# Optimization experiments

Measured on AMD Instinct MI355X. Metric: run time of the kernel, lower is better.

The kernel has to match this reference:

```python
import jax, jax.numpy as jnp
import numpy as np

N, E, H, B = 100000, 1600000, 64, 256
EPS = 1e-5


def ln(x, g, b):
    mu = jnp.mean(x, axis=-1, keepdims=True)
    var = jnp.mean((x - mu) ** 2, axis=-1, keepdims=True)
    return (x - mu) * jax.lax.rsqrt(var + EPS) * g + b


def gelu(x):
    # torch nn.GELU default is exact (erf) gelu
    return jax.nn.gelu(x, approximate=False)


def setup_inputs() -> dict:
    key = jax.random.key(0)
    ks = iter(jax.random.split(key, 64))
    nk = lambda: next(ks)
    s = 0.1
    p = {}
    p["x"] = jax.random.normal(nk(), (N, 2), jnp.float32)
    p["edge_attr"] = jax.random.normal(nk(), (E, 2), jnp.float32)
    # node_embed: Linear(2,H) LN GELU Linear(H,H) LN GELU (dropout = eval no-op)
    p["ne_w1"] = jax.random.normal(nk(), (2, H), jnp.float32) * s
    p["ne_b1"] = jnp.zeros((H,), jnp.float32)
    p["ne_g1"] = jnp.ones((H,), jnp.float32)
    p["ne_be1"] = jnp.zeros((H,), jnp.float32)
    p["ne_w2"] = jax.random.normal(nk(), (H, H), jnp.float32) * s
    p["ne_b2"] = jnp.zeros((H,), jnp.float32)
    p["ne_g2"] = jnp.ones((H,), jnp.float32)
    p["ne_be2"] = jnp.zeros((H,), jnp.float32)
    # 3 TrackConv layers: message MLP Linear(H+2,H)+LN, conv output LN, and outer per-layer LN
    p["conv_w"] = jax.random.normal(nk(), (3, H + 2, H), jnp.float32) * s
    p["conv_b"] = jnp.zeros((3, H), jnp.float32)
    p["conv_mg"] = jnp.ones((3, H), jnp.float32)
    p["conv_mb"] = jnp.zeros((3, H), jnp.float32)
    p["conv_ng"] = jnp.ones((3, H), jnp.float32)
    p["conv_nb"] = jnp.zeros((3, H), jnp.float32)
    p["out_ng"] = jnp.ones((3, H), jnp.float32)
    p["out_nb"] = jnp.zeros((3, H), jnp.float32)
    # head MLP: Linear(H,H)+LN+ReLU, Linear(H,H//2)+LN+ReLU, Linear(H//2,1)
    p["m_w1"] = jax.random.normal(nk(), (H, H), jnp.float32) * s
    p["m_b1"] = jnp.zeros((H,), jnp.float32)
    p["m_g1"] = jnp.ones((H,), jnp.float32)
    p["m_be1"] = jnp.zeros((H,), jnp.float32)
    p["m_w2"] = jax.random.normal(nk(), (H, H // 2), jnp.float32) * s
    p["m_b2"] = jnp.zeros((H // 2,), jnp.float32)
    p["m_g2"] = jnp.ones((H // 2,), jnp.float32)
    p["m_be2"] = jnp.zeros((H // 2,), jnp.float32)
    p["m_w3"] = jax.random.normal(nk(), (H // 2, 1), jnp.float32) * s
    p["m_b3"] = jnp.zeros((1,), jnp.float32)
    p["edge_index"] = jax.random.randint(nk(), (2, E), 0, N, dtype=jnp.int32)
    p["batch"] = jnp.sort(jax.random.randint(nk(), (N,), 0, B, dtype=jnp.int32))
    return p


def reference(x, edge_attr,
              ne_w1, ne_b1, ne_g1, ne_be1, ne_w2, ne_b2, ne_g2, ne_be2,
              conv_w, conv_b, conv_mg, conv_mb, conv_ng, conv_nb, out_ng, out_nb,
              m_w1, m_b1, m_g1, m_be1, m_w2, m_b2, m_g2, m_be2, m_w3, m_b3,
              edge_index, batch):
    # node embedding (dropout in eval = identity)
    h = gelu(ln(x @ ne_w1 + ne_b1, ne_g1, ne_be1))
    h = gelu(ln(h @ ne_w2 + ne_b2, ne_g2, ne_be2))
    src, dst = edge_index[0], edge_index[1]  # PyG: message from src (x_j), aggregate at dst
    deg = jax.ops.segment_sum(jnp.ones((E,), h.dtype), dst, num_segments=N)
    deg = jnp.maximum(deg, 1.0)[:, None]
    for l in range(3):
        msg_in = jnp.concatenate([h[src], edge_attr], axis=-1)  # [E, H+2]
        msg = gelu(ln(msg_in @ conv_w[l] + conv_b[l], conv_mg[l], conv_mb[l]))  # [E, H]
        agg = jax.ops.segment_sum(msg, dst, num_segments=N) / deg  # mean aggregate
        conv_out = ln(agg + h, conv_ng[l], conv_nb[l])  # TrackConv: norm(out + residual)
        h = h + ln(conv_out, out_ng[l], out_nb[l])  # outer norm + residual
    # global mean pool over graphs
    cnt = jnp.maximum(jax.ops.segment_sum(jnp.ones((N,), h.dtype), batch, num_segments=B), 1.0)[:, None]
    g = jax.ops.segment_sum(h, batch, num_segments=B) / cnt  # [B, H]
    g = jax.nn.relu(ln(g @ m_w1 + m_b1, m_g1, m_be1))
    g = jax.nn.relu(ln(g @ m_w2 + m_b2, m_g2, m_be2))
    return g @ m_w3 + m_b3  # [B, 1]
```

## Files before the change

### kernel.cpp

```cpp
#include <hip/hip_runtime.h>
#include <math.h>


typedef __attribute__((ext_vector_type(8))) short bfrag;
typedef __attribute__((ext_vector_type(4))) float ffrag;

template <int CTRL>
__device__ __forceinline__ float dpp_mov(float v) {
  return __int_as_float(
      __builtin_amdgcn_update_dpp(0, __float_as_int(v), CTRL, 0xF, 0xF, true));
}

__device__ __forceinline__ float rsum16(float v) {
  v += dpp_mov<0x128>(v);
  v += dpp_mov<0x124>(v);
  v += dpp_mov<0x122>(v);
  v += dpp_mov<0x121>(v);
  return v;
}

__device__ __forceinline__ float wave_sum64(float v) {
  v = rsum16(v);
  v += __shfl_xor(v, 16, 64);
  v += __shfl_xor(v, 32, 64);
  return v;
}

__device__ __forceinline__ float ln_apply(float t, float g, float b) {
  float s1 = wave_sum64(t);
  float s2 = wave_sum64(t * t);
  float mu = s1 * 0.015625f;
  float var = fmaf(-mu, mu, s2 * 0.015625f);
  return (t - mu) * rsqrtf(var + 1e-5f) * g + b;
}

__device__ __forceinline__ float erf_fast(float x) {
  float ax = fabsf(x);
  float p = fmaf(fmaf(fmaf(fmaf(0.078108f, ax, 0.000972f), ax, 0.230389f),
                      ax, 0.278393f), ax, 1.0f);
  p = p * p;
  p = p * p;
  float r = __builtin_amdgcn_rcpf(p);
  return copysignf(1.0f - r, x);
}

__device__ __forceinline__ float gelu_exact(float v) {
  float half = 0.5f * v;
  return fmaf(half, erf_fast(v * 0.70710678118654752440f), half);
}

__device__ __forceinline__ float lane_bcast(float v, int k) {
  return __uint_as_float(__builtin_amdgcn_readlane(__float_as_uint(v), k));
}

__device__ __forceinline__ short f2bf(float f) {
  union { float f; unsigned u; } v; v.f = f;
  unsigned r = v.u + 0x7fffu + ((v.u >> 16) & 1u);
  return (short)(r >> 16);
}

__global__ __launch_bounds__(256) void k_init1(
    const float* __restrict__ conv_w, ushort* __restrict__ wt,
    const int* __restrict__ ei, int* __restrict__ csr,
    int ne, int oHist) {
  const int bid = blockIdx.x;
  const int tid = threadIdx.x;
  if (bid < oHist) {
    const int i = bid * 256 + tid;
    const int k = i % 96, f = (i / 96) % 64, l = i / (96 * 64);
    const float v = (k < 66) ? conv_w[(size_t)l * 66 * 64 + k * 64 + f] : 0.0f;
    wt[i] = (ushort)f2bf(v);
    return;
  }
  const int i = (bid - oHist) * 256 + tid;
  if (i < ne) atomicAdd(&csr[__builtin_nontemporal_load(ei + ne + i)], 1);
}

__global__ __launch_bounds__(1024) void k_scan_fast(int* __restrict__ buf, int n) {
  __shared__ int wsum[16];
  const int tid = threadIdx.x, lane = tid & 63, w = tid >> 6;
  const int chunk = (((n + 1023) / 1024) + 3) & ~3;
  const int a = min(tid * chunk, n), b = min(a + chunk, n);
  const bool full = (a + chunk <= n);
  int s = 0;
  if (full) {
    const int4* p4 = (const int4*)(buf + a);
#pragma unroll 4
    for (int i = 0; i < chunk / 4; i++) {
      int4 v = p4[i];
      s += v.x + v.y + v.z + v.w;
    }
  } else {
    for (int i = a; i < b; i++) s += buf[i];
  }
  int inc = s;
#pragma unroll
  for (int sh = 1; sh < 64; sh <<= 1) {
    int t = __shfl_up(inc, sh, 64);
    if (lane >= sh) inc += t;
  }
  if (lane == 63) wsum[w] = inc;
  __syncthreads();
  int wb = 0;
  for (int j = 0; j < w; j++) wb += wsum[j];
  int excl = wb + inc - s;
  if (full) {
    int4* p4 = (int4*)(buf + a);
#pragma unroll 4
    for (int i = 0; i < chunk / 4; i++) {
      int4 v = p4[i];
      int4 o;
      o.x = excl; excl += v.x;
      o.y = excl; excl += v.y;
      o.z = excl; excl += v.z;
      o.w = excl; excl += v.w;
      p4[i] = o;
    }
  } else {
    for (int i = a; i < b; i++) { int v = buf[i]; buf[i] = excl; excl += v; }
  }
}

__global__ __launch_bounds__(256) void k_combo(
    const int* __restrict__ ei, const float* __restrict__ ea,
    int* __restrict__ cursor, int4* __restrict__ edata,
    const float* __restrict__ x,
    const float* __restrict__ w1, const float* __restrict__ b1,
    const float* __restrict__ g1, const float* __restrict__ be1,
    const float* __restrict__ w2, const float* __restrict__ b2,
    const float* __restrict__ g2, const float* __restrict__ be2,
    float* __restrict__ h, ushort* __restrict__ hb,
    int n_nodes, int ne, int nOrd, int embWaves, float roleScale) {
  const int bid = blockIdx.x;
  const int tid = threadIdx.x;
  const int sub = bid & 31;
  if (sub < 24) {
    const int role = bid & 7;
    const int ord = (bid >> 5) * 3 + (sub >> 3);
    const int lo = (int)((long long)ord * ne / nOrd);
    const int hi = (int)((long long)(ord + 1) * ne / nOrd);
    for (int i = lo + tid; i < hi; i += 256) {
      const int d = __builtin_nontemporal_load(ei + ne + i);
      const int rd = min(7, (int)((float)d * roleScale));
      if (rd == role) {
        const int s = __builtin_nontemporal_load(ei + i);
        const unsigned long long eau =
            __builtin_nontemporal_load((const unsigned long long*)ea + i);
        const float e0 = __uint_as_float((unsigned)eau);
        const float e1 = __uint_as_float((unsigned)(eau >> 32));
        const unsigned pk = (unsigned)(ushort)f2bf(e0) |
                            ((unsigned)(ushort)f2bf(e1) << 16);
        const int pos = atomicAdd(&cursor[d], 1);
        edata[pos] = make_int4(s, (int)pk, d, 0);
      }
    }
    return;
  }
  const int lane = tid & 63;
  const int eblk = (bid >> 5) * 8 + (sub - 24);
  const int wid = (eblk * 256 + tid) >> 6;
  const int nw = embWaves;
  float wc[64];
#pragma unroll
  for (int k = 0; k < 64; k++) wc[k] = w2[k * 64 + lane];
  const float w1a = w1[lane], w1b = w1[64 + lane];
  const float vb1 = b1[lane], vg1 = g1[lane], vbe1 = be1[lane];
  const float vb2 = b2[lane], vg2 = g2[lane], vbe2 = be2[lane];
  for (int n = wid; n < n_nodes; n += nw) {
    const float x0 = x[2 * n], x1 = x[2 * n + 1];
    float t = fmaf(x0, w1a, fmaf(x1, w1b, vb1));
    t = gelu_exact(ln_apply(t, vg1, vbe1));
    float a0 = vb2, a1 = 0.f, a2 = 0.f, a3 = 0.f;
#pragma unroll
    for (int k = 0; k < 64; k += 4) {
      a0 = fmaf(lane_bcast(t, k + 0), wc[k + 0], a0);
      a1 = fmaf(lane_bcast(t, k + 1), wc[k + 1], a1);
      a2 = fmaf(lane_bcast(t, k + 2), wc[k + 2], a2);
      a3 = fmaf(lane_bcast(t, k + 3), wc[k + 3], a3);
    }
    float acc = (a0 + a1) + (a2 + a3);
    acc = gelu_exact(ln_apply(acc, vg2, vbe2));
    __builtin_nontemporal_store(acc, h + (size_t)n * 64 + lane);
    __builtin_nontemporal_store((ushort)f2bf(acc),
                                hb + (size_t)n * 64 + lane);
  }
}

__global__ __launch_bounds__(256, 3) void k_edge_packed(
    const ushort* __restrict__ hb_in, float* __restrict__ agg,
    const int4* __restrict__ edata, const ushort* __restrict__ wt,
    const float* __restrict__ bias, const float* __restrict__ mg,
    const float* __restrict__ mb, int nchunks, int ne) {
  __shared__ __align__(16) ushort lwt[64 * 96];
  {
    const uint4* s = (const uint4*)wt;
    uint4* d = (uint4*)lwt;
    for (int i = threadIdx.x; i < 768; i += 256) d[i] = s[i];
  }
  __syncthreads();

  const int lane = threadIdx.x & 63;
  const int grp = lane >> 4, col = lane & 15;
  const int wid = (blockIdx.x * blockDim.x + threadIdx.x) >> 6;
  const int nw = (gridDim.x * blockDim.x) >> 6;

  float vb[4], vg[4], vbb[4];
#pragma unroll
  for (int t = 0; t < 4; t++) {
    const int f = t * 16 + col;
    vb[t] = bias[f]; vg[t] = mg[f]; vbb[t] = mb[f];
  }

  int c = wid;
  if (c >= nchunks) return;
  int4 e = edata[min(16 * c + col, ne - 1)];
  const ushort* hp0 = hb_in + (size_t)e.x * 64 + grp * 8;
  bfrag A0 = *(const bfrag*)(hp0);
  bfrag A1 = *(const bfrag*)(hp0 + 32);

  for (;;) {
    const int rem = min(16, ne - 16 * c);
    const int cn = c + nw;
    const bool more = cn < nchunks;
    const int nslot = more ? min(16 * cn + col, ne - 1) : min(16 * c + col, ne - 1);
    const int4 en = edata[nslot];

    bfrag A2 = {0, 0, 0, 0, 0, 0, 0, 0};
    if (grp == 0) {
      A2[0] = (short)(e.y & 0xffff);
      A2[1] = (short)((unsigned)e.y >> 16);
    }

    ffrag acc[4];
#pragma unroll
    for (int t = 0; t < 4; t++) { ffrag cc = {vb[t], vb[t], vb[t], vb[t]}; acc[t] = cc; }
#pragma unroll
    for (int t = 0; t < 4; t++) {
      const bfrag B = *(const bfrag*)(lwt + (t * 16 + col) * 96 + grp * 8);
      acc[t] = __builtin_amdgcn_mfma_f32_16x16x32_bf16(A0, B, acc[t], 0, 0, 0);
    }
#pragma unroll
    for (int t = 0; t < 4; t++) {
      const bfrag B = *(const bfrag*)(lwt + (t * 16 + col) * 96 + 32 + grp * 8);
      acc[t] = __builtin_amdgcn_mfma_f32_16x16x32_bf16(A1, B, acc[t], 0, 0, 0);
    }
#pragma unroll
    for (int t = 0; t < 4; t++) {
      const bfrag B = *(const bfrag*)(lwt + (t * 16 + col) * 96 + 64 + grp * 8);
      acc[t] = __builtin_amdgcn_mfma_f32_16x16x32_bf16(A2, B, acc[t], 0, 0, 0);
    }

    const ushort* hq = hb_in + (size_t)en.x * 64 + grp * 8;
    const bfrag N0 = *(const bfrag*)(hq);
    const bfrag N1 = *(const bfrag*)(hq + 32);

    float sx[4], sq[4];
#pragma unroll
    for (int r = 0; r < 4; r++) {
      float s = (acc[0][r] + acc[1][r]) + (acc[2][r] + acc[3][r]);
      float q = fmaf(acc[0][r], acc[0][r], fmaf(acc[1][r], acc[1][r],
                fmaf(acc[2][r], acc[2][r], acc[3][r] * acc[3][r])));
      sx[r] = s; sq[r] = q;
    }
#pragma unroll
    for (int r = 0; r < 4; r++) sx[r] = rsum16(sx[r]);
#pragma unroll
    for (int r = 0; r < 4; r++) sq[r] = rsum16(sq[r]);
    float iv[4], mi[4];
#pragma unroll
    for (int r = 0; r < 4; r++) {
      const float mu = sx[r] * 0.015625f;
      const float var = fmaf(-mu, mu, sq[r] * 0.015625f);
      iv[r] = rsqrtf(var + 1e-5f);
      mi[r] = -mu * iv[r];
    }

#pragma unroll
    for (int t = 0; t < 4; t++) {
#pragma unroll
      for (int r = 0; r < 4; r++) {
        const float z = fmaf(acc[t][r], iv[r], mi[r]);
        acc[t][r] = gelu_exact(fmaf(z, vg[t], vbb[t]));
      }
    }

    const int prev = __shfl_up(e.z, 1, 64);
    const unsigned long long bal = __ballot((col > 0) && (e.z != prev));
    const unsigned bm = (unsigned)bal & 0xFFFEu;

    int s0 = 0;
    while (s0 < rem) {
      const unsigned rest = bm >> (s0 + 1);
      int s1 = rest ? (s0 + 1 + __builtin_ctz(rest)) : 16;
      if (s1 > rem) s1 = rem;
      const int dseg = __builtin_amdgcn_readlane(e.z, s0);
#pragma unroll
      for (int t = 0; t < 4; t++) {
        float rs = 0.f;
#pragma unroll
        for (int r = 0; r < 4; r++) {
          const int row = grp * 4 + r;
          const float w = (row >= s0 && row < s1) ? 1.0f : 0.0f;
          rs = fmaf(acc[t][r], w, rs);
        }
        rs += __shfl_xor(rs, 16, 64);
        rs += __shfl_xor(rs, 32, 64);
        if (lane < 16)
          atomicAdd(&agg[(size_t)dseg * 64 + t * 16 + lane], rs);
      }
      s0 = s1;
    }

    if (!more) break;
    c = cn; e = en; A0 = N0; A1 = N1;
  }
}

__global__ void k_node_update(float* __restrict__ h, ushort* __restrict__ hb,
                              float* __restrict__ agg, const int* __restrict__ ends,
                              const float* __restrict__ ng, const float* __restrict__ nb,
                              const float* __restrict__ og, const float* __restrict__ ob,
                              int n_nodes, int writeHb) {
  const int lane = threadIdx.x & 63;
  const int n = (blockIdx.x * blockDim.x + threadIdx.x) >> 6;
  if (n >= n_nodes) return;
  int start, end;
  if (n == 0) { start = 0; end = ends[0]; }
  else { const int2 se = *(const int2*)(ends + n - 1); start = se.x; end = se.y; }
  const float dg = fmaxf((float)(end - start), 1.0f);
  const float hv = h[(size_t)n * 64 + lane];
  const float a = agg[(size_t)n * 64 + lane] / dg + hv;
  if (writeHb) agg[(size_t)n * 64 + lane] = 0.0f;
  const float c = ln_apply(a, ng[lane], nb[lane]);
  const float o = ln_apply(c, og[lane], ob[lane]);
  const float outv = hv + o;
  h[(size_t)n * 64 + lane] = outv;
  if (writeHb) hb[(size_t)n * 64 + lane] = (ushort)f2bf(outv);
}

__global__ void k_pool_seg(const float* __restrict__ h, const int* __restrict__ batch,
                           float* __restrict__ g, float* __restrict__ cnt,
                           int n_nodes, int chunk) {
  const int lane = threadIdx.x & 63;
  const int wid = (blockIdx.x * blockDim.x + threadIdx.x) >> 6;
  const int n0 = wid * chunk;
  if (n0 >= n_nodes) return;
  const int n1 = min(n0 + chunk, n_nodes);
  int cur = batch[n0], c = 0;
  float acc = 0.f;
  for (int n = n0; n < n1; n++) {
    const int b = batch[n];
    if (b != cur) {
      atomicAdd(&g[(size_t)cur * 64 + lane], acc);
      if (lane == 0) atomicAdd(&cnt[cur], (float)c);
      acc = 0.f; c = 0; cur = b;
    }
    acc += h[(size_t)n * 64 + lane];
    c++;
  }
  atomicAdd(&g[(size_t)cur * 64 + lane], acc);
  if (lane == 0) atomicAdd(&cnt[cur], (float)c);
}

__global__ void k_head(const float* __restrict__ g, const float* __restrict__ cnt,
                       const float* __restrict__ w1, const float* __restrict__ b1,
                       const float* __restrict__ g1, const float* __restrict__ be1,
                       const float* __restrict__ w2, const float* __restrict__ b2,
                       const float* __restrict__ g2, const float* __restrict__ be2,
                       const float* __restrict__ w3, const float* __restrict__ b3,
                       float* __restrict__ out, int nb_) {
  const int lane = threadIdx.x & 63;
  const int row = (blockIdx.x * blockDim.x + threadIdx.x) >> 6;
  if (row >= nb_) return;
  const float c = fmaxf(cnt[row], 1.0f);
  const float gv = g[row * 64 + lane] / c;
  float a0 = b1[lane], a1 = 0.f, a2 = 0.f, a3 = 0.f;
#pragma unroll
  for (int k = 0; k < 64; k += 4) {
    a0 = fmaf(lane_bcast(gv, k + 0), w1[(k + 0) * 64 + lane], a0);
    a1 = fmaf(lane_bcast(gv, k + 1), w1[(k + 1) * 64 + lane], a1);
    a2 = fmaf(lane_bcast(gv, k + 2), w1[(k + 2) * 64 + lane], a2);
    a3 = fmaf(lane_bcast(gv, k + 3), w1[(k + 3) * 64 + lane], a3);
  }
  float t = (a0 + a1) + (a2 + a3);
  t = fmaxf(ln_apply(t, g1[lane], be1[lane]), 0.0f);

  const int j = lane & 31;
  float c0 = b2[j], c1 = 0.f, c2 = 0.f, c3 = 0.f;
#pragma unroll
  for (int k = 0; k < 64; k += 4) {
    c0 = fmaf(lane_bcast(t, k + 0), w2[(k + 0) * 32 + j], c0);
    c1 = fmaf(lane_bcast(t, k + 1), w2[(k + 1) * 32 + j], c1);
    c2 = fmaf(lane_bcast(t, k + 2), w2[(k + 2) * 32 + j], c2);
    c3 = fmaf(lane_bcast(t, k + 3), w2[(k + 3) * 32 + j], c3);
  }
  float t2 = (c0 + c1) + (c2 + c3);
  t2 = fmaxf(ln_apply(t2, g2[j], be2[j]), 0.0f);
  const float p = t2 * w3[j];
  const float s = wave_sum64(p) * 0.5f;
  if (lane == 0) out[row] = s + b3[0];
}

extern "C" void kernel_launch(void* const* d_in, const int* in_sizes, int n_in,
                              void* d_out, int out_size, void* d_ws, size_t ws_size,
                              hipStream_t stream) {
  const float* x      = (const float*)d_in[0];
  const float* ea     = (const float*)d_in[1];
  const float* ne_w1  = (const float*)d_in[2];
  const float* ne_b1  = (const float*)d_in[3];
  const float* ne_g1  = (const float*)d_in[4];
  const float* ne_be1 = (const float*)d_in[5];
  const float* ne_w2  = (const float*)d_in[6];
  const float* ne_b2  = (const float*)d_in[7];
  const float* ne_g2  = (const float*)d_in[8];
  const float* ne_be2 = (const float*)d_in[9];
  const float* conv_w = (const float*)d_in[10];
  const float* conv_b = (const float*)d_in[11];
  const float* conv_mg= (const float*)d_in[12];
  const float* conv_mb= (const float*)d_in[13];
  const float* conv_ng= (const float*)d_in[14];
  const float* conv_nb= (const float*)d_in[15];
  const float* out_ng = (const float*)d_in[16];
  const float* out_nb = (const float*)d_in[17];
  const float* m_w1   = (const float*)d_in[18];
  const float* m_b1   = (const float*)d_in[19];
  const float* m_g1   = (const float*)d_in[20];
  const float* m_be1  = (const float*)d_in[21];
  const float* m_w2   = (const float*)d_in[22];
  const float* m_b2   = (const float*)d_in[23];
  const float* m_g2   = (const float*)d_in[24];
  const float* m_be2  = (const float*)d_in[25];
  const float* m_w3   = (const float*)d_in[26];
  const float* m_b3   = (const float*)d_in[27];
  const int*   eidx   = (const int*)d_in[28];
  const int*   batch  = (const int*)d_in[29];
  float* outp = (float*)d_out;

  const int NN = in_sizes[29];
  const int NE = in_sizes[1] / 2;
  const int NB = out_size;
  const int NCH = (NE + 15) / 16;

  char* wsb = (char*)d_ws;
  float*  h    = (float*)wsb;
  ushort* hb   = (ushort*)(h + (size_t)NN * 64);
  int4*   edata= (int4*)((char*)hb + ((size_t)NN * 128 + 15) / 16 * 16);
  ushort* wt   = (ushort*)(edata + NE);
  float*  gbuf = (float*)(wt + 3 * 64 * 96);
  float*  cnt  = gbuf + (size_t)NB * 64;
  int*    csr  = (int*)(cnt + NB);
  float*  agg  = (float*)((char*)(csr + NN) +
                          (((size_t)(uintptr_t)(csr + NN) & 15) ? 16 - ((size_t)(uintptr_t)(csr + NN) & 15) : 0));

  const dim3 blk(256);

  const size_t zbytes = (char*)(agg + (size_t)NN * 64) - (char*)gbuf;
  hipMemsetAsync(gbuf, 0, zbytes, stream);

  const int nPrep = (3 * 64 * 96) / 256;
  const int nHist = (NE + 255) / 256;
  k_init1<<<nPrep + nHist, blk, 0, stream>>>(conv_w, wt, eidx, csr, NE, nPrep);

  k_scan_fast<<<1, 1024, 0, stream>>>(csr, NN);

  const int ngroups = 261;
  const int nOrd = ngroups * 3;
  const int nEmb = ngroups * 8;
  k_combo<<<ngroups * 32, blk, 0, stream>>>(
      eidx, ea, csr, edata, x,
      ne_w1, ne_b1, ne_g1, ne_be1, ne_w2, ne_b2, ne_g2, ne_be2,
      h, hb, NN, NE, nOrd, nEmb * 4, 8.0f / (float)NN);

  for (int l = 0; l < 3; l++) {
    k_edge_packed<<<4096, blk, 0, stream>>>(
        hb, agg, edata, wt + (size_t)l * 64 * 96,
        conv_b + l * 64, conv_mg + l * 64, conv_mb + l * 64, NCH, NE);
    k_node_update<<<(NN * 64 + 255) / 256, blk, 0, stream>>>(
        h, hb, agg, csr, conv_ng + l * 64, conv_nb + l * 64,
        out_ng + l * 64, out_nb + l * 64, NN, (l < 2) ? 1 : 0);
  }

  {
    const int chunk = 32;
    const int nwaves = (NN + chunk - 1) / chunk;
    const int nblocks = (nwaves * 64 + 255) / 256;
    k_pool_seg<<<nblocks, blk, 0, stream>>>(h, batch, gbuf, cnt, NN, chunk);
  }
  k_head<<<(NB + 3) / 4, blk, 0, stream>>>(gbuf, cnt, m_w1, m_b1, m_g1, m_be1,
                                           m_w2, m_b2, m_g2, m_be2, m_w3, m_b3,
                                           outp, NB);
}
```

Before: 744.6 us.

## Partition edges by destination node ranges to replace atomics with plain stores

Each wave now owns a contiguous range of destination nodes, found by binary search over the CSR offsets, so the edges it processes are split at node boundaries. Partial sums for a destination that spans chunks are carried in registers and written once with a plain store instead of atomicAdd. This drops the float atomics and the zeroing of the aggregation buffer each layer, and the memset no longer covers agg. In exchange, work per wave is uneven when node degrees are skewed, and each wave pays for two binary searches.

```diff
diff --git a/kernel.cpp b/kernel.cpp
--- a/kernel.cpp
+++ b/kernel.cpp
@@ -4,6 +4,8 @@
 
 typedef __attribute__((ext_vector_type(8))) short bfrag;
 typedef __attribute__((ext_vector_type(4))) float ffrag;
+
+#define NWV 16384
 
 template <int CTRL>
 __device__ __forceinline__ float dpp_mov(float v) {
@@ -57,6 +59,16 @@
   union { float f; unsigned u; } v; v.f = f;
   unsigned r = v.u + 0x7fffu + ((v.u >> 16) & 1u);
   return (short)(r >> 16);
+}
+
+__device__ __forceinline__ int ub_search(const int* __restrict__ a, int n,
+                                         long long T) {
+  int lo = 0, hi = n;
+  while (lo < hi) {
+    const int mid = (lo + hi) >> 1;
+    if ((long long)a[mid] > T) hi = mid; else lo = mid + 1;
+  }
+  return lo;
 }
 
 __global__ __launch_bounds__(256) void k_init1(
@@ -186,11 +198,12 @@
   }
 }
 
-__global__ __launch_bounds__(256, 3) void k_edge_packed(
+__global__ __launch_bounds__(256, 3) void k_edge_seq(
     const ushort* __restrict__ hb_in, float* __restrict__ agg,
-    const int4* __restrict__ edata, const ushort* __restrict__ wt,
+    const int4* __restrict__ edata, const int* __restrict__ csr,
+    const ushort* __restrict__ wt,
     const float* __restrict__ bias, const float* __restrict__ mg,
-    const float* __restrict__ mb, int nchunks, int ne) {
+    const float* __restrict__ mb, int nn, int ne) {
   __shared__ __align__(16) ushort lwt[64 * 96];
   {
     const uint4* s = (const uint4*)wt;
@@ -200,9 +213,18 @@
   __syncthreads();
 
   const int lane = threadIdx.x & 63;
+  const int wgl = (int)((blockIdx.x * blockDim.x + threadIdx.x) >> 6);
+  const long long Ta = (long long)wgl * ne / NWV;
+  const long long Tb = (long long)(wgl + 1) * ne / NWV;
+  const int n0 = ub_search(csr, nn, Ta);
+  const int n1 = (wgl + 1 == NWV) ? nn : ub_search(csr, nn, Tb);
+  if (n0 >= n1) return;
+  const int e_lo = (n0 > 0) ? csr[n0 - 1] : 0;
+  const int e_hi = csr[n1 - 1];
+  const int nch = (e_hi - e_lo + 15) >> 4;
+  if (nch == 0) return;
+
   const int grp = lane >> 4, col = lane & 15;
-  const int wid = (blockIdx.x * blockDim.x + threadIdx.x) >> 6;
-  const int nw = (gridDim.x * blockDim.x) >> 6;
 
   float vb[4], vg[4], vbb[4];
 #pragma unroll
@@ -211,18 +233,18 @@
     vb[t] = bias[f]; vg[t] = mg[f]; vbb[t] = mb[f];
   }
 
-  int c = wid;
-  if (c >= nchunks) return;
-  int4 e = edata[min(16 * c + col, ne - 1)];
+  float car[4] = {0.f, 0.f, 0.f, 0.f};
+
+  int slot = min(e_lo + col, e_hi - 1);
+  int4 e = edata[slot];
   const ushort* hp0 = hb_in + (size_t)e.x * 64 + grp * 8;
   bfrag A0 = *(const bfrag*)(hp0);
   bfrag A1 = *(const bfrag*)(hp0 + 32);
 
-  for (;;) {
-    const int rem = min(16, ne - 16 * c);
-    const int cn = c + nw;
-    const bool more = cn < nchunks;
-    const int nslot = more ? min(16 * cn + col, ne - 1) : min(16 * c + col, ne - 1);
+  for (int c = 0;;) {
+    const int rem = min(16, e_hi - e_lo - 16 * c);
+    const bool more = (c + 1) < nch;
+    const int nslot = more ? min(e_lo + 16 * (c + 1) + col, e_hi - 1) : slot;
     const int4 en = edata[nslot];
 
     bfrag A2 = {0, 0, 0, 0, 0, 0, 0, 0};
@@ -287,6 +309,7 @@
     const int prev = __shfl_up(e.z, 1, 64);
     const unsigned long long bal = __ballot((col > 0) && (e.z != prev));
     const unsigned bm = (unsigned)bal & 0xFFFEu;
+    const int peek = more ? __builtin_amdgcn_readlane(en.z, 0) : -1;
 
     int s0 = 0;
     while (s0 < rem) {
@@ -294,30 +317,44 @@
       int s1 = rest ? (s0 + 1 + __builtin_ctz(rest)) : 16;
       if (s1 > rem) s1 = rem;
       const int dseg = __builtin_amdgcn_readlane(e.z, s0);
+
+      float rs[4];
 #pragma unroll
       for (int t = 0; t < 4; t++) {
-        float rs = 0.f;
+        float r_ = 0.f;
 #pragma unroll
         for (int r = 0; r < 4; r++) {
           const int row = grp * 4 + r;
           const float w = (row >= s0 && row < s1) ? 1.0f : 0.0f;
-          rs = fmaf(acc[t][r], w, rs);
+          r_ = fmaf(acc[t][r], w, r_);
         }
-        rs += __shfl_xor(rs, 16, 64);
-        rs += __shfl_xor(rs, 32, 64);
-        if (lane < 16)
-          atomicAdd(&agg[(size_t)dseg * 64 + t * 16 + lane], rs);
+        r_ += __shfl_xor(r_, 16, 64);
+        r_ += __shfl_xor(r_, 32, 64);
+        rs[t] = r_;
+      }
+
+      const bool comp = (s1 < rem) || (!more) || (peek != dseg);
+      if (comp) {
+        if (lane < 16) {
+#pragma unroll
+          for (int t = 0; t < 4; t++)
+            agg[(size_t)dseg * 64 + t * 16 + lane] = car[t] + rs[t];
+        }
+        car[0] = car[1] = car[2] = car[3] = 0.f;
+      } else {
+#pragma unroll
+        for (int t = 0; t < 4; t++) car[t] += rs[t];
       }
       s0 = s1;
     }
 
     if (!more) break;
-    c = cn; e = en; A0 = N0; A1 = N1;
+    c++; slot = nslot; e = en; A0 = N0; A1 = N1;
   }
 }
 
 __global__ void k_node_update(float* __restrict__ h, ushort* __restrict__ hb,
-                              float* __restrict__ agg, const int* __restrict__ ends,
+                              const float* __restrict__ agg, const int* __restrict__ ends,
                               const float* __restrict__ ng, const float* __restrict__ nb,
                               const float* __restrict__ og, const float* __restrict__ ob,
                               int n_nodes, int writeHb) {
@@ -329,8 +366,8 @@
   else { const int2 se = *(const int2*)(ends + n - 1); start = se.x; end = se.y; }
   const float dg = fmaxf((float)(end - start), 1.0f);
   const float hv = h[(size_t)n * 64 + lane];
-  const float a = agg[(size_t)n * 64 + lane] / dg + hv;
-  if (writeHb) agg[(size_t)n * 64 + lane] = 0.0f;
+  const float av = (end > start) ? agg[(size_t)n * 64 + lane] : 0.0f;
+  const float a = av / dg + hv;
   const float c = ln_apply(a, ng[lane], nb[lane]);
   const float o = ln_apply(c, og[lane], ob[lane]);
   const float outv = hv + o;
@@ -439,7 +476,6 @@
   const int NN = in_sizes[29];
   const int NE = in_sizes[1] / 2;
   const int NB = out_size;
-  const int NCH = (NE + 15) / 16;
 
   char* wsb = (char*)d_ws;
   float*  h    = (float*)wsb;
@@ -454,7 +490,7 @@
 
   const dim3 blk(256);
 
-  const size_t zbytes = (char*)(agg + (size_t)NN * 64) - (char*)gbuf;
+  const size_t zbytes = (char*)(csr + NN) - (char*)gbuf;
   hipMemsetAsync(gbuf, 0, zbytes, stream);
 
   const int nPrep = (3 * 64 * 96) / 256;
@@ -472,9 +508,9 @@
       h, hb, NN, NE, nOrd, nEmb * 4, 8.0f / (float)NN);
 
   for (int l = 0; l < 3; l++) {
-    k_edge_packed<<<4096, blk, 0, stream>>>(
-        hb, agg, edata, wt + (size_t)l * 64 * 96,
-        conv_b + l * 64, conv_mg + l * 64, conv_mb + l * 64, NCH, NE);
+    k_edge_seq<<<NWV / 4, blk, 0, stream>>>(
+        hb, agg, edata, csr, wt + (size_t)l * 64 * 96,
+        conv_b + l * 64, conv_mg + l * 64, conv_mb + l * 64, NN, NE);
     k_node_update<<<(NN * 64 + 255) / 256, blk, 0, stream>>>(
         h, hb, agg, csr, conv_ng + l * 64, conv_nb + l * 64,
         out_ng + l * 64, out_nb + l * 64, NN, (l < 2) ? 1 : 0);
```

Result: slower. 827.6 us (+11.1%).
